# Kernel tuning notes

Measured on AMD Instinct MI355X. Metric: run time of the kernel, lower is better.

Reference implementation:

```python
import jax, jax.numpy as jnp
import numpy as np

D_MODEL = 1024
N_HEADS = 16
HEAD_DIM = D_MODEL // N_HEADS
NEG_INF = -1e10


def setup_inputs() -> dict:
    key = jax.random.key(0)
    ks = jax.random.split(key, 6)
    B, S = 2, 2048
    x = jax.random.normal(ks[0], (B, S, D_MODEL), dtype=jnp.float32)
    mask = jnp.ones((B, S), dtype=jnp.int32)
    scale_w = 1.0 / np.sqrt(D_MODEL)
    Wq = jax.random.normal(ks[1], (D_MODEL, D_MODEL), dtype=jnp.float32) * scale_w
    Wk = jax.random.normal(ks[2], (D_MODEL, D_MODEL), dtype=jnp.float32) * scale_w
    Wv = jax.random.normal(ks[3], (D_MODEL, D_MODEL), dtype=jnp.float32) * scale_w
    Wo = jax.random.normal(ks[4], (D_MODEL, D_MODEL), dtype=jnp.float32) * scale_w
    bq = jnp.zeros((D_MODEL,), jnp.float32)
    bk = jnp.zeros((D_MODEL,), jnp.float32)
    bv = jnp.zeros((D_MODEL,), jnp.float32)
    bo = jnp.zeros((D_MODEL,), jnp.float32)
    return {"x": x, "mask": mask, "Wq": Wq, "bq": bq, "Wk": Wk, "bk": bk,
            "Wv": Wv, "bv": bv, "Wo": Wo, "bo": bo}


def reference(x, mask, Wq, bq, Wk, bk, Wv, bv, Wo, bo):
    B, S, _ = x.shape
    # Linear projections (torch Linear: y = x @ W.T + b)
    Q = x @ Wq.T + bq
    K = x @ Wk.T + bk
    V = x @ Wv.T + bv
    # [B, H, S, Dh]
    Q = Q.reshape(B, S, N_HEADS, HEAD_DIM).transpose(0, 2, 1, 3)
    K = K.reshape(B, S, N_HEADS, HEAD_DIM).transpose(0, 2, 1, 3)
    V = V.reshape(B, S, N_HEADS, HEAD_DIM).transpose(0, 2, 1, 3)
    scale = jnp.sqrt(jnp.float32(HEAD_DIM))
    energy = jnp.einsum('bhqd,bhkd->bhqk', Q, K) / scale  # [B,H,S,S]
    # mask: [B,S] -> broadcast over heads and query dim (keys masked)
    m = mask[:, None, None, :]  # [B,1,1,S]
    energy = jnp.where(m == 0, jnp.float32(NEG_INF), energy)
    attention = jax.nn.softmax(energy, axis=-1)
    # dropout in eval mode = identity
    out = jnp.einsum('bhqk,bhkd->bhqd', attention, V)  # [B,H,S,Dh]
    out = out.transpose(0, 2, 1, 3).reshape(B, S, D_MODEL)
    return out @ Wo.T + bo
```

## Files before the change

kernel.cpp:

```cpp
#include <hip/hip_runtime.h>
#include <hip/hip_bf16.h>

typedef __hip_bfloat16 bf16;
typedef __attribute__((ext_vector_type(8))) short s8v;
typedef __attribute__((ext_vector_type(4))) float f4v;

#define D_MODEL 1024
#define S_LEN   2048
#define BATCH   2
#define NH      16
#define HD      64
#define M_TOTAL 4096
#define NT      (S_LEN / 64)

__device__ __forceinline__ void gll16(const bf16* g, bf16* l) {
    __builtin_amdgcn_global_load_lds(
        (const __attribute__((address_space(1))) void*)g,
        (__attribute__((address_space(3))) void*)l, 16, 0, 0);
}

struct CvtPtrs {
    const float* sx; bf16* dx;
    const float* s0; const float* s1; const float* s2; const float* s3;
    bf16* d0; bf16* d1; bf16* d2; bf16* d3;
};

__global__ __launch_bounds__(256) void cvt_all(CvtPtrs p) {
    const int bid = blockIdx.x;
    const float* s; bf16* d; int i;
    if (bid < 2048) {
        s = p.sx; d = p.dx;
        i = (bid * 256 + threadIdx.x) * 8;
    } else {
        const int wsel = (bid - 2048) >> 9;
        const int wb   = (bid - 2048) & 511;
        s = (wsel == 0) ? p.s0 : (wsel == 1) ? p.s1 : (wsel == 2) ? p.s2 : p.s3;
        d = (wsel == 0) ? p.d0 : (wsel == 1) ? p.d1 : (wsel == 2) ? p.d2 : p.d3;
        i = (wb * 256 + threadIdx.x) * 8;
    }
    float4 a = *(const float4*)(s + i);
    float4 b = *(const float4*)(s + i + 4);
    union { bf16 h[8]; uint4 u; } q;
    q.h[0] = __float2bfloat16(a.x); q.h[1] = __float2bfloat16(a.y);
    q.h[2] = __float2bfloat16(a.z); q.h[3] = __float2bfloat16(a.w);
    q.h[4] = __float2bfloat16(b.x); q.h[5] = __float2bfloat16(b.y);
    q.h[6] = __float2bfloat16(b.z); q.h[7] = __float2bfloat16(b.w);
    *(uint4*)(d + i) = q.u;
}

template<int TM, int TN>
__device__ __forceinline__ void gemm_main(const bf16* __restrict__ A,
                                          const bf16* __restrict__ W,
                                          bf16* As, bf16* Bs,
                                          int bm, int bn,
                                          f4v (&acc)[TM/32][TN/32])
{
    constexpr int FM = TM / 32, FN = TN / 32;
    constexpr int CALLS_A = TM / 16, CALLS = (TM + TN) / 16, PW = CALLS / 4;
    const int t = threadIdx.x, wv = t >> 6, lane = t & 63;
    const int quad = lane >> 4, l15 = lane & 15;
    const int wm = (wv >> 1) * (TM / 2), wn = (wv & 1) * (TN / 2);
    const int lr = lane >> 2, lc = (lane & 3) * 8;

    auto STAGE = [&](int buf, int k0) {
        #pragma unroll
        for (int c = 0; c < PW; ++c) {
            const int cc = wv * PW + c;
            if (cc < CALLS_A) {
                gll16(A + (size_t)(bm + cc * 16 + lr) * D_MODEL + k0 + lc,
                      As + buf * (TM * 32) + cc * 16 * 32);
            } else {
                const int r2 = cc - CALLS_A;
                gll16(W + (size_t)(bn + r2 * 16 + lr) * D_MODEL + k0 + lc,
                      Bs + buf * (TN * 32) + r2 * 16 * 32);
            }
        }
    };

    STAGE(0, 0);
    __syncthreads();
    int cur = 0;

    for (int k0 = 0; k0 < D_MODEL; k0 += 32) {
        if (k0 + 32 < D_MODEL) STAGE(cur ^ 1, k0 + 32);

        const bf16* ab = As + cur * (TM * 32);
        const bf16* bb = Bs + cur * (TN * 32);
        s8v af[FM], bfv[FN];
        #pragma unroll
        for (int i = 0; i < FM; ++i)
            af[i] = *(const s8v*)(ab + (wm + i * 16 + l15) * 32 + quad * 8);
        #pragma unroll
        for (int j = 0; j < FN; ++j)
            bfv[j] = *(const s8v*)(bb + (wn + j * 16 + l15) * 32 + quad * 8);
        __builtin_amdgcn_s_setprio(1);
        #pragma unroll
        for (int i = 0; i < FM; ++i)
            #pragma unroll
            for (int j = 0; j < FN; ++j)
                acc[i][j] = __builtin_amdgcn_mfma_f32_16x16x32_bf16(af[i], bfv[j], acc[i][j], 0, 0, 0);
        __builtin_amdgcn_s_setprio(0);

        __syncthreads();
        cur ^= 1;
    }
}

__global__ __launch_bounds__(256) void gemm_qkv(
    const bf16* __restrict__ x,
    const bf16* __restrict__ Wq, const bf16* __restrict__ Wk, const bf16* __restrict__ Wv,
    const float* __restrict__ bq, const float* __restrict__ bk, const float* __restrict__ bv,
    bf16* __restrict__ Qb, bf16* __restrict__ Kb, bf16* __restrict__ Vtb)
{
    __shared__ __align__(16) char smem[4 * 64 * 72 * 2];
    bf16* As = (bf16*)smem;
    bf16* Bs = (bf16*)(smem + 2 * 128 * 32 * 2);
    bf16 (*Tw)[64][72] = (bf16(*)[64][72])smem;

    const int z = blockIdx.z;
    const bf16*  W    = (z == 0) ? Wq : (z == 1) ? Wk : Wv;
    const float* bias = (z == 0) ? bq : (z == 1) ? bk : bv;
    bf16*        out  = (z == 0) ? Qb : (z == 1) ? Kb : Vtb;
    const int bm = blockIdx.y * 128, bn = blockIdx.x * 128;

    f4v acc[4][4] = {};
    gemm_main<128, 128>(x, W, As, Bs, bm, bn, acc);

    const int t = threadIdx.x, wv = t >> 6, lane = t & 63;
    const int quad = lane >> 4, l15 = lane & 15;
    const int wm = (wv >> 1) * 64, wn = (wv & 1) * 64;

    if (z == 2) {
        __syncthreads();
        #pragma unroll
        for (int j = 0; j < 4; ++j) {
            const int col = bn + wn + j * 16 + l15;
            const float bv_ = bias[col];
            #pragma unroll
            for (int i = 0; i < 4; ++i) {
                #pragma unroll
                for (int rp = 0; rp < 4; rp += 2) {
                    union { bf16 h[2]; unsigned u; } p2;
                    p2.h[0] = __float2bfloat16(acc[i][j][rp]     + bv_);
                    p2.h[1] = __float2bfloat16(acc[i][j][rp + 1] + bv_);
                    *(unsigned*)&Tw[wv][j * 16 + l15][i * 16 + quad * 4 + rp] = p2.u;
                }
            }
        }
        const int bb = (bm + wm) >> 11, s0 = (bm + wm) & 2047;
        #pragma unroll
        for (int p = 0; p < 8; ++p) {
            const int dl = p * 8 + (lane >> 3);
            const int sl = (lane & 7) * 8;
            const int col = bn + wn + dl;
            const int h = col >> 6, d = col & 63;
            uint4 v = *(const uint4*)&Tw[wv][dl][sl];
            *(uint4*)&out[(((size_t)(bb * NH + h)) * HD + d) * S_LEN + s0 + sl] = v;
        }
    } else {
        #pragma unroll
        for (int j = 0; j < 4; ++j) {
            const int col = bn + wn + j * 16 + l15;
            const float bv_ = bias[col];
            const int h = col >> 6, d = col & 63;
            #pragma unroll
            for (int i = 0; i < 4; ++i) {
                #pragma unroll
                for (int r = 0; r < 4; ++r) {
                    const int row = bm + wm + i * 16 + quad * 4 + r;
                    const int b = row >> 11, s = row & 2047;
                    const float v = acc[i][j][r] + bv_;
                    out[(((size_t)(b * NH + h)) * S_LEN + s) * HD + d] = __float2bfloat16(v);
                }
            }
        }
    }
}

__global__ __launch_bounds__(256) void gemm_out(
    const bf16* __restrict__ Ob, const bf16* __restrict__ Wo,
    const float* __restrict__ bo, float* __restrict__ out)
{
    __shared__ __align__(16) bf16 As[2][64 * 32];
    __shared__ __align__(16) bf16 Bs[2][128 * 32];
    const int bm = blockIdx.y * 64, bn = blockIdx.x * 128;

    f4v acc[2][4] = {};
    gemm_main<64, 128>(Ob, Wo, &As[0][0], &Bs[0][0], bm, bn, acc);

    const int t = threadIdx.x, wv = t >> 6, lane = t & 63;
    const int quad = lane >> 4, l15 = lane & 15;
    const int wm = (wv >> 1) * 32, wn = (wv & 1) * 64;
    #pragma unroll
    for (int j = 0; j < 4; ++j) {
        const int col = bn + wn + j * 16 + l15;
        const float bv_ = bo[col];
        #pragma unroll
        for (int i = 0; i < 2; ++i)
            #pragma unroll
            for (int r = 0; r < 4; ++r) {
                const int row = bm + wm + i * 16 + quad * 4 + r;
                out[(size_t)row * D_MODEL + col] = acc[i][j][r] + bv_;
            }
    }
}

__global__ __launch_bounds__(256) void attn_mfma(
    const bf16* __restrict__ Q, const bf16* __restrict__ K,
    const bf16* __restrict__ Vt, const int* __restrict__ mask,
    bf16* __restrict__ O)
{
    __shared__ __align__(16) bf16 Ks[64][64];
    __shared__ __align__(16) bf16 Vts[64][64];
    __shared__ __align__(16) bf16 Ps[4][16][64];
    __shared__ __align__(16) float mbias[S_LEN];

    const int t = threadIdx.x, wv = t >> 6, lane = t & 63;
    const int quad = lane >> 4, l15 = lane & 15;
    const int sw = l15 & 7;
    const int bid = blockIdx.x;
    const int b = bid & 1, h = (bid >> 1) & 15, qt = bid >> 5;
    const int q0 = qt * 64;
    const size_t qkbase = ((size_t)(b * NH + h)) * S_LEN * HD;
    const size_t vtbase = ((size_t)(b * NH + h)) * HD * S_LEN;

    const float KSC  = 0.125f * 1.44269504f;
    const float THR2 = 8.0f * 1.44269504f;

    const bf16* qrow = Q + qkbase + (size_t)(q0 + wv * 16 + l15) * HD;
    const s8v qf0 = *(const s8v*)(qrow + quad * 8);
    const s8v qf1 = *(const s8v*)(qrow + 32 + quad * 8);

    #pragma unroll
    for (int i = 0; i < S_LEN / 256; ++i) {
        const int idx = i * 256 + t;
        mbias[idx] = mask[b * S_LEN + idx] ? 0.f : -1e30f;
    }

    const int srow = t >> 2;
    const int swr  = srow & 7;
    const int c2   = (t & 3) * 2;
    const int ch0  = c2 ^ swr, ch1 = (c2 + 1) ^ swr;

    uint4 kr0, kr1, vr0, vr1;
    auto LOADT = [&](int kt2) {
        const int kk = kt2 * 64;
        const uint4* kp = (const uint4*)(K  + qkbase + (size_t)(kk + srow) * HD + c2 * 8);
        const uint4* vp = (const uint4*)(Vt + vtbase + (size_t)srow * S_LEN + kk + c2 * 8);
        kr0 = kp[0]; kr1 = kp[1];
        vr0 = vp[0]; vr1 = vp[1];
    };
    auto STAGE = [&]() {
        *(uint4*)&Ks[srow][ch0 * 8]  = kr0;
        *(uint4*)&Ks[srow][ch1 * 8]  = kr1;
        *(uint4*)&Vts[srow][ch0 * 8] = vr0;
        *(uint4*)&Vts[srow][ch1 * 8] = vr1;
    };

    LOADT(0);

    float mprev = -1e30f, lsum = 0.f;
    f4v oacc[4] = {};

    for (int kt = 0; kt < NT; ++kt) {
        const int k0 = kt * 64;
        __syncthreads();
        STAGE();
        __syncthreads();
        if (kt + 1 < NT) LOADT(kt + 1);

        f4v st[4];
        __builtin_amdgcn_s_setprio(1);
        #pragma unroll
        for (int c = 0; c < 4; ++c) {
            const char* kr = (const char*)&Ks[c * 16 + l15][0];
            s8v kf0 = *(const s8v*)(kr + ((quad ^ sw) << 4));
            s8v kf1 = *(const s8v*)(kr + (((4 + quad) ^ sw) << 4));
            f4v z = {0.f, 0.f, 0.f, 0.f};
            z = __builtin_amdgcn_mfma_f32_16x16x32_bf16(kf0, qf0, z, 0, 0, 0);
            z = __builtin_amdgcn_mfma_f32_16x16x32_bf16(kf1, qf1, z, 0, 0, 0);
            st[c] = z;
        }
        __builtin_amdgcn_s_setprio(0);

        float mt = -1e30f;
        #pragma unroll
        for (int c = 0; c < 4; ++c) {
            const f4v m4 = *(const f4v*)&mbias[k0 + c * 16 + quad * 4];
            st[c] = st[c] * KSC + m4;
            mt = fmaxf(mt, fmaxf(fmaxf(st[c][0], st[c][1]), fmaxf(st[c][2], st[c][3])));
        }
        mt = fmaxf(mt, __shfl_xor(mt, 16, 64));
        mt = fmaxf(mt, __shfl_xor(mt, 32, 64));

        float mn = mprev;
        if (!__all(mt <= mprev + THR2)) {
            mn = fmaxf(mprev, mt);
            const float alpha = __builtin_amdgcn_exp2f(mprev - mn);
            mprev = mn;
            float av[4];
            #pragma unroll
            for (int r = 0; r < 4; ++r) av[r] = __shfl(alpha, quad * 4 + r, 64);
            #pragma unroll
            for (int dt = 0; dt < 4; ++dt)
                #pragma unroll
                for (int r = 0; r < 4; ++r) oacc[dt][r] *= av[r];
            lsum *= alpha;
        }

        f4v psv = {0.f, 0.f, 0.f, 0.f};
        #pragma unroll
        for (int c = 0; c < 4; ++c) {
            f4v e = st[c] - mn;
            e[0] = __builtin_amdgcn_exp2f(e[0]);
            e[1] = __builtin_amdgcn_exp2f(e[1]);
            e[2] = __builtin_amdgcn_exp2f(e[2]);
            e[3] = __builtin_amdgcn_exp2f(e[3]);
            st[c] = e;
            psv += e;
        }
        lsum += psv[0] + psv[1] + psv[2] + psv[3];

        char* pr = (char*)&Ps[wv][l15][0];
        #pragma unroll
        for (int c = 0; c < 4; ++c) {
            union { bf16 hh[4]; short4 s4; } pk;
            pk.hh[0] = __float2bfloat16(st[c][0]);
            pk.hh[1] = __float2bfloat16(st[c][1]);
            pk.hh[2] = __float2bfloat16(st[c][2]);
            pk.hh[3] = __float2bfloat16(st[c][3]);
            const int wch = (2 * c + (quad >> 1)) ^ sw;
            *(short4*)(pr + (wch << 4) + ((quad & 1) << 3)) = pk.s4;
        }
        s8v pf0 = *(const s8v*)(pr + ((quad ^ sw) << 4));
        s8v pf1 = *(const s8v*)(pr + (((4 + quad) ^ sw) << 4));

        __builtin_amdgcn_s_setprio(1);
        #pragma unroll
        for (int dt = 0; dt < 4; ++dt) {
            const char* vr = (const char*)&Vts[dt * 16 + l15][0];
            s8v vf0 = *(const s8v*)(vr + ((quad ^ sw) << 4));
            s8v vf1 = *(const s8v*)(vr + (((4 + quad) ^ sw) << 4));
            oacc[dt] = __builtin_amdgcn_mfma_f32_16x16x32_bf16(pf0, vf0, oacc[dt], 0, 0, 0);
            oacc[dt] = __builtin_amdgcn_mfma_f32_16x16x32_bf16(pf1, vf1, oacc[dt], 0, 0, 0);
        }
        __builtin_amdgcn_s_setprio(0);
    }

    lsum += __shfl_xor(lsum, 16, 64);
    lsum += __shfl_xor(lsum, 32, 64);
    float linv[4];
    #pragma unroll
    for (int r = 0; r < 4; ++r) linv[r] = 1.f / __shfl(lsum, quad * 4 + r, 64);
    #pragma unroll
    for (int dt = 0; dt < 4; ++dt) {
        #pragma unroll
        for (int r = 0; r < 4; ++r) {
            const int s = q0 + wv * 16 + quad * 4 + r;
            const int col = h * 64 + dt * 16 + l15;
            O[((size_t)b * S_LEN + s) * D_MODEL + col] = __float2bfloat16(oacc[dt][r] * linv[r]);
        }
    }
}

extern "C" void kernel_launch(void* const* d_in, const int* in_sizes, int n_in,
                              void* d_out, int out_size, void* d_ws, size_t ws_size,
                              hipStream_t stream) {
    const float* x    = (const float*)d_in[0];
    const int*   mask = (const int*)  d_in[1];
    const float* Wq   = (const float*)d_in[2];
    const float* bq   = (const float*)d_in[3];
    const float* Wk   = (const float*)d_in[4];
    const float* bk   = (const float*)d_in[5];
    const float* Wv   = (const float*)d_in[6];
    const float* bv   = (const float*)d_in[7];
    const float* Wo   = (const float*)d_in[8];
    const float* bo   = (const float*)d_in[9];
    float* out = (float*)d_out;

    char* w = (char*)d_ws;
    bf16* xb  = (bf16*)w; w += (size_t)M_TOTAL * D_MODEL * 2;
    bf16* Wqb = (bf16*)w; w += (size_t)D_MODEL * D_MODEL * 2;
    bf16* Wkb = (bf16*)w; w += (size_t)D_MODEL * D_MODEL * 2;
    bf16* Wvb = (bf16*)w; w += (size_t)D_MODEL * D_MODEL * 2;
    bf16* Wob = (bf16*)w; w += (size_t)D_MODEL * D_MODEL * 2;
    bf16* Qb  = (bf16*)w; w += (size_t)M_TOTAL * D_MODEL * 2;
    bf16* Kb  = (bf16*)w; w += (size_t)M_TOTAL * D_MODEL * 2;
    bf16* Vtb = (bf16*)w; w += (size_t)M_TOTAL * D_MODEL * 2;
    bf16* Ob  = (bf16*)w; w += (size_t)M_TOTAL * D_MODEL * 2;

    CvtPtrs cp = { x, xb, Wq, Wk, Wv, Wo, Wqb, Wkb, Wvb, Wob };
    cvt_all<<<4096, 256, 0, stream>>>(cp);

    gemm_qkv<<<dim3(8, 32, 3), 256, 0, stream>>>(xb, Wqb, Wkb, Wvb, bq, bk, bv, Qb, Kb, Vtb);

    attn_mfma<<<BATCH * NH * (S_LEN / 64), 256, 0, stream>>>(Qb, Kb, Vtb, mask, Ob);

    gemm_out<<<dim3(8, 64), 256, 0, stream>>>(Ob, Wob, bo, out);
}
```

Measured before the change: 210.3 us.

## Process two 16-row query tiles per wave in attention to reuse K/V tiles

Each wave now handles 32 query rows instead of 16, so a block covers 128 queries and the grid is halved. Every K/V tile staged into shared memory and every K/V fragment read from LDS now feeds twice as many MFMAs, which cuts global K/V traffic and LDS reads per unit of work. In exchange, register pressure rises from the duplicated accumulators and softmax state, and the grid drops to 512 blocks, which may hurt occupancy and load balance across CUs.

```diff
diff --git a/kernel.cpp b/kernel.cpp
--- a/kernel.cpp
+++ b/kernel.cpp
@@ -212,7 +212,7 @@
 {
     __shared__ __align__(16) bf16 Ks[64][64];
     __shared__ __align__(16) bf16 Vts[64][64];
-    __shared__ __align__(16) bf16 Ps[4][16][64];
+    __shared__ __align__(16) bf16 Ps[4][32][64];
     __shared__ __align__(16) float mbias[S_LEN];
 
     const int t = threadIdx.x, wv = t >> 6, lane = t & 63;
@@ -220,16 +220,19 @@
     const int sw = l15 & 7;
     const int bid = blockIdx.x;
     const int b = bid & 1, h = (bid >> 1) & 15, qt = bid >> 5;
-    const int q0 = qt * 64;
+    const int q0 = qt * 128;
     const size_t qkbase = ((size_t)(b * NH + h)) * S_LEN * HD;
     const size_t vtbase = ((size_t)(b * NH + h)) * HD * S_LEN;
 
     const float KSC  = 0.125f * 1.44269504f;
     const float THR2 = 8.0f * 1.44269504f;
 
-    const bf16* qrow = Q + qkbase + (size_t)(q0 + wv * 16 + l15) * HD;
-    const s8v qf0 = *(const s8v*)(qrow + quad * 8);
-    const s8v qf1 = *(const s8v*)(qrow + 32 + quad * 8);
+    const bf16* qrow0 = Q + qkbase + (size_t)(q0 + wv * 32 + l15) * HD;
+    const bf16* qrow1 = qrow0 + (size_t)16 * HD;
+    const s8v qf0 = *(const s8v*)(qrow0 + quad * 8);
+    const s8v qf1 = *(const s8v*)(qrow0 + 32 + quad * 8);
+    const s8v qf2 = *(const s8v*)(qrow1 + quad * 8);
+    const s8v qf3 = *(const s8v*)(qrow1 + 32 + quad * 8);
 
     #pragma unroll
     for (int i = 0; i < S_LEN / 256; ++i) {
@@ -259,8 +262,10 @@
 
     LOADT(0);
 
-    float mprev = -1e30f, lsum = 0.f;
-    f4v oacc[4] = {};
+    float mprev0 = -1e30f, lsum0 = 0.f;
+    float mprev1 = -1e30f, lsum1 = 0.f;
+    f4v oacc0[4] = {};
+    f4v oacc1[4] = {};
 
     for (int kt = 0; kt < NT; ++kt) {
         const int k0 = kt * 64;
@@ -269,71 +274,107 @@
         __syncthreads();
         if (kt + 1 < NT) LOADT(kt + 1);
 
-        f4v st[4];
+        f4v st0[4], st1[4];
         __builtin_amdgcn_s_setprio(1);
         #pragma unroll
         for (int c = 0; c < 4; ++c) {
             const char* kr = (const char*)&Ks[c * 16 + l15][0];
             s8v kf0 = *(const s8v*)(kr + ((quad ^ sw) << 4));
             s8v kf1 = *(const s8v*)(kr + (((4 + quad) ^ sw) << 4));
-            f4v z = {0.f, 0.f, 0.f, 0.f};
-            z = __builtin_amdgcn_mfma_f32_16x16x32_bf16(kf0, qf0, z, 0, 0, 0);
-            z = __builtin_amdgcn_mfma_f32_16x16x32_bf16(kf1, qf1, z, 0, 0, 0);
-            st[c] = z;
+            f4v z0 = {0.f, 0.f, 0.f, 0.f};
+            z0 = __builtin_amdgcn_mfma_f32_16x16x32_bf16(kf0, qf0, z0, 0, 0, 0);
+            z0 = __builtin_amdgcn_mfma_f32_16x16x32_bf16(kf1, qf1, z0, 0, 0, 0);
+            st0[c] = z0;
+            f4v z1 = {0.f, 0.f, 0.f, 0.f};
+            z1 = __builtin_amdgcn_mfma_f32_16x16x32_bf16(kf0, qf2, z1, 0, 0, 0);
+            z1 = __builtin_amdgcn_mfma_f32_16x16x32_bf16(kf1, qf3, z1, 0, 0, 0);
+            st1[c] = z1;
         }
         __builtin_amdgcn_s_setprio(0);
 
-        float mt = -1e30f;
+        float mt0 = -1e30f, mt1 = -1e30f;
         #pragma unroll
         for (int c = 0; c < 4; ++c) {
             const f4v m4 = *(const f4v*)&mbias[k0 + c * 16 + quad * 4];
-            st[c] = st[c] * KSC + m4;
-            mt = fmaxf(mt, fmaxf(fmaxf(st[c][0], st[c][1]), fmaxf(st[c][2], st[c][3])));
-        }
-        mt = fmaxf(mt, __shfl_xor(mt, 16, 64));
-        mt = fmaxf(mt, __shfl_xor(mt, 32, 64));
-
-        float mn = mprev;
-        if (!__all(mt <= mprev + THR2)) {
-            mn = fmaxf(mprev, mt);
-            const float alpha = __builtin_amdgcn_exp2f(mprev - mn);
-            mprev = mn;
+            st0[c] = st0[c] * KSC + m4;
+            st1[c] = st1[c] * KSC + m4;
+            mt0 = fmaxf(mt0, fmaxf(fmaxf(st0[c][0], st0[c][1]), fmaxf(st0[c][2], st0[c][3])));
+            mt1 = fmaxf(mt1, fmaxf(fmaxf(st1[c][0], st1[c][1]), fmaxf(st1[c][2], st1[c][3])));
+        }
+        mt0 = fmaxf(mt0, __shfl_xor(mt0, 16, 64));
+        mt0 = fmaxf(mt0, __shfl_xor(mt0, 32, 64));
+        mt1 = fmaxf(mt1, __shfl_xor(mt1, 16, 64));
+        mt1 = fmaxf(mt1, __shfl_xor(mt1, 32, 64));
+
+        float mn0 = mprev0;
+        if (!__all(mt0 <= mprev0 + THR2)) {
+            mn0 = fmaxf(mprev0, mt0);
+            const float alpha = __builtin_amdgcn_exp2f(mprev0 - mn0);
+            mprev0 = mn0;
             float av[4];
             #pragma unroll
             for (int r = 0; r < 4; ++r) av[r] = __shfl(alpha, quad * 4 + r, 64);
             #pragma unroll
             for (int dt = 0; dt < 4; ++dt)
                 #pragma unroll
-                for (int r = 0; r < 4; ++r) oacc[dt][r] *= av[r];
-            lsum *= alpha;
-        }
-
-        f4v psv = {0.f, 0.f, 0.f, 0.f};
+                for (int r = 0; r < 4; ++r) oacc0[dt][r] *= av[r];
+            lsum0 *= alpha;
+        }
+        float mn1 = mprev1;
+        if (!__all(mt1 <= mprev1 + THR2)) {
+            mn1 = fmaxf(mprev1, mt1);
+            const float alpha = __builtin_amdgcn_exp2f(mprev1 - mn1);
+            mprev1 = mn1;
+            float av[4];
+            #pragma unroll
+            for (int r = 0; r < 4; ++r) av[r] = __shfl(alpha, quad * 4 + r, 64);
+            #pragma unroll
+            for (int dt = 0; dt < 4; ++dt)
+                #pragma unroll
+                for (int r = 0; r < 4; ++r) oacc1[dt][r] *= av[r];
+            lsum1 *= alpha;
+        }
+
+        f4v ps0 = {0.f, 0.f, 0.f, 0.f}, ps1 = {0.f, 0.f, 0.f, 0.f};
         #pragma unroll
         for (int c = 0; c < 4; ++c) {
-            f4v e = st[c] - mn;
-            e[0] = __builtin_amdgcn_exp2f(e[0]);
-            e[1] = __builtin_amdgcn_exp2f(e[1]);
-            e[2] = __builtin_amdgcn_exp2f(e[2]);
-            e[3] = __builtin_amdgcn_exp2f(e[3]);
-            st[c] = e;
-            psv += e;
-        }
-        lsum += psv[0] + psv[1] + psv[2] + psv[3];
-
-        char* pr = (char*)&Ps[wv][l15][0];
+            f4v e0 = st0[c] - mn0;
+            e0[0] = __builtin_amdgcn_exp2f(e0[0]);
+            e0[1] = __builtin_amdgcn_exp2f(e0[1]);
+            e0[2] = __builtin_amdgcn_exp2f(e0[2]);
+            e0[3] = __builtin_amdgcn_exp2f(e0[3]);
+            st0[c] = e0; ps0 += e0;
+            f4v e1 = st1[c] - mn1;
+            e1[0] = __builtin_amdgcn_exp2f(e1[0]);
+            e1[1] = __builtin_amdgcn_exp2f(e1[1]);
+            e1[2] = __builtin_amdgcn_exp2f(e1[2]);
+            e1[3] = __builtin_amdgcn_exp2f(e1[3]);
+            st1[c] = e1; ps1 += e1;
+        }
+        lsum0 += ps0[0] + ps0[1] + ps0[2] + ps0[3];
+        lsum1 += ps1[0] + ps1[1] + ps1[2] + ps1[3];
+
+        char* pr0 = (char*)&Ps[wv][l15][0];
+        char* pr1 = (char*)&Ps[wv][16 + l15][0];
         #pragma unroll
         for (int c = 0; c < 4; ++c) {
-            union { bf16 hh[4]; short4 s4; } pk;
-            pk.hh[0] = __float2bfloat16(st[c][0]);
-            pk.hh[1] = __float2bfloat16(st[c][1]);
-            pk.hh[2] = __float2bfloat16(st[c][2]);
-            pk.hh[3] = __float2bfloat16(st[c][3]);
+            union { bf16 hh[4]; short4 s4; } pk0, pk1;
+            pk0.hh[0] = __float2bfloat16(st0[c][0]);
+            pk0.hh[1] = __float2bfloat16(st0[c][1]);
+            pk0.hh[2] = __float2bfloat16(st0[c][2]);
+            pk0.hh[3] = __float2bfloat16(st0[c][3]);
+            pk1.hh[0] = __float2bfloat16(st1[c][0]);
+            pk1.hh[1] = __float2bfloat16(st1[c][1]);
+            pk1.hh[2] = __float2bfloat16(st1[c][2]);
+            pk1.hh[3] = __float2bfloat16(st1[c][3]);
             const int wch = (2 * c + (quad >> 1)) ^ sw;
-            *(short4*)(pr + (wch << 4) + ((quad & 1) << 3)) = pk.s4;
-        }
-        s8v pf0 = *(const s8v*)(pr + ((quad ^ sw) << 4));
-        s8v pf1 = *(const s8v*)(pr + (((4 + quad) ^ sw) << 4));
+            *(short4*)(pr0 + (wch << 4) + ((quad & 1) << 3)) = pk0.s4;
+            *(short4*)(pr1 + (wch << 4) + ((quad & 1) << 3)) = pk1.s4;
+        }
+        s8v pfA0 = *(const s8v*)(pr0 + ((quad ^ sw) << 4));
+        s8v pfA1 = *(const s8v*)(pr0 + (((4 + quad) ^ sw) << 4));
+        s8v pfB0 = *(const s8v*)(pr1 + ((quad ^ sw) << 4));
+        s8v pfB1 = *(const s8v*)(pr1 + (((4 + quad) ^ sw) << 4));
 
         __builtin_amdgcn_s_setprio(1);
         #pragma unroll
@@ -341,24 +382,36 @@
             const char* vr = (const char*)&Vts[dt * 16 + l15][0];
             s8v vf0 = *(const s8v*)(vr + ((quad ^ sw) << 4));
             s8v vf1 = *(const s8v*)(vr + (((4 + quad) ^ sw) << 4));
-            oacc[dt] = __builtin_amdgcn_mfma_f32_16x16x32_bf16(pf0, vf0, oacc[dt], 0, 0, 0);
-            oacc[dt] = __builtin_amdgcn_mfma_f32_16x16x32_bf16(pf1, vf1, oacc[dt], 0, 0, 0);
+            oacc0[dt] = __builtin_amdgcn_mfma_f32_16x16x32_bf16(pfA0, vf0, oacc0[dt], 0, 0, 0);
+            oacc0[dt] = __builtin_amdgcn_mfma_f32_16x16x32_bf16(pfA1, vf1, oacc0[dt], 0, 0, 0);
+            oacc1[dt] = __builtin_amdgcn_mfma_f32_16x16x32_bf16(pfB0, vf0, oacc1[dt], 0, 0, 0);
+            oacc1[dt] = __builtin_amdgcn_mfma_f32_16x16x32_bf16(pfB1, vf1, oacc1[dt], 0, 0, 0);
         }
         __builtin_amdgcn_s_setprio(0);
     }
 
-    lsum += __shfl_xor(lsum, 16, 64);
-    lsum += __shfl_xor(lsum, 32, 64);
-    float linv[4];
+    lsum0 += __shfl_xor(lsum0, 16, 64);
+    lsum0 += __shfl_xor(lsum0, 32, 64);
+    lsum1 += __shfl_xor(lsum1, 16, 64);
+    lsum1 += __shfl_xor(lsum1, 32, 64);
+    float linv0[4], linv1[4];
     #pragma unroll
-    for (int r = 0; r < 4; ++r) linv[r] = 1.f / __shfl(lsum, quad * 4 + r, 64);
+    for (int r = 0; r < 4; ++r) {
+        linv0[r] = 1.f / __shfl(lsum0, quad * 4 + r, 64);
+        linv1[r] = 1.f / __shfl(lsum1, quad * 4 + r, 64);
+    }
+    const int sbase = q0 + wv * 32;
     #pragma unroll
     for (int dt = 0; dt < 4; ++dt) {
+        const int col = h * 64 + dt * 16 + l15;
         #pragma unroll
         for (int r = 0; r < 4; ++r) {
-            const int s = q0 + wv * 16 + quad * 4 + r;
-            const int col = h * 64 + dt * 16 + l15;
-            O[((size_t)b * S_LEN + s) * D_MODEL + col] = __float2bfloat16(oacc[dt][r] * linv[r]);
+            const int s0r = sbase + quad * 4 + r;
+            O[((size_t)b * S_LEN + s0r) * D_MODEL + col] =
+                __float2bfloat16(oacc0[dt][r] * linv0[r]);
+            const int s1r = sbase + 16 + quad * 4 + r;
+            O[((size_t)b * S_LEN + s1r) * D_MODEL + col] =
+                __float2bfloat16(oacc1[dt][r] * linv1[r]);
         }
     }
 }
@@ -394,7 +447,7 @@
 
     gemm_qkv<<<dim3(8, 32, 3), 256, 0, stream>>>(xb, Wqb, Wkb, Wvb, bq, bk, bv, Qb, Kb, Vtb);
 
-    attn_mfma<<<BATCH * NH * (S_LEN / 64), 256, 0, stream>>>(Qb, Kb, Vtb, mask, Ob);
+    attn_mfma<<<BATCH * NH * (S_LEN / 128), 256, 0, stream>>>(Qb, Kb, Vtb, mask, Ob);
 
     gemm_out<<<dim3(8, 64), 256, 0, stream>>>(Ob, Wob, bo, out);
 }
```

Measured after the change: 210.6 us. About the same (+0.2%).
